# Optimization experiments

Hardware: AMD Instinct MI355X
Metric: run time of the kernel (lower is better)

The kernel has to match this reference:

```python
import jax, jax.numpy as jnp
import numpy as np

N = 8192          # total proposals
D_IN = 256 * 7 * 7  # 12544
HID = 1024
C = 3


def setup_inputs() -> dict:
    key = jax.random.key(0)
    ks = jax.random.split(key, 9)
    s_in = 1.0 / np.sqrt(D_IN)
    s_h = 1.0 / np.sqrt(HID)
    return {
        "feature_vectors": jax.random.normal(ks[0], (N, D_IN), dtype=jnp.float32),
        "W1": jax.random.uniform(ks[1], (D_IN, HID), jnp.float32, -s_in, s_in),
        "b1": jax.random.uniform(ks[2], (HID,), jnp.float32, -s_in, s_in),
        "W2": jax.random.uniform(ks[3], (HID, HID), jnp.float32, -s_h, s_h),
        "b2": jax.random.uniform(ks[4], (HID,), jnp.float32, -s_h, s_h),
        "Wc": jax.random.uniform(ks[5], (HID, C + 1), jnp.float32, -s_h, s_h),
        "bc": jax.random.uniform(ks[6], (C + 1,), jnp.float32, -s_h, s_h),
        "Wr": jax.random.uniform(ks[7], (HID, 4 * C), jnp.float32, -s_h, s_h),
        "br": jax.random.uniform(ks[8], (4 * C,), jnp.float32, -s_h, s_h),
    }


def reference(feature_vectors, W1, b1, W2, b2, Wc, bc, Wr, br):
    # intermediate: Linear -> Linear -> ReLU (note: no ReLU between the two Linears,
    # matching the original nn.Sequential ordering)
    h = feature_vectors @ W1 + b1          # [N, 1024]
    h = h @ W2 + b2                        # [N, 1024]
    h = jax.nn.relu(h)
    class_logits = jax.nn.softmax(h @ Wc + bc, axis=-1)  # [N, C+1]
    box_pred = h @ Wr + br                  # [N, 4C]
    return class_logits, box_pred
```

## Files before the change

kernel.cpp:

```cpp
#include <hip/hip_runtime.h>
#include <hip/hip_bf16.h>
#include <stdint.h>

using u16 = unsigned short;
using u32 = unsigned int;

typedef __attribute__((ext_vector_type(8))) short short8;
typedef __attribute__((ext_vector_type(4))) float floatx4;

__device__ __forceinline__ u16 f2bf(float f) {
  __hip_bfloat16 h = __float2bfloat16(f);
  return *reinterpret_cast<u16*>(&h);
}

__device__ __forceinline__ void gl_lds16(const void* g, void* l) {
  __builtin_amdgcn_global_load_lds((const __attribute__((address_space(1))) void*)g,
                                   (__attribute__((address_space(3))) void*)l, 16, 0, 0);
}

__global__ __launch_bounds__(256)
void transpose_to_bf16(const float* __restrict__ in, u16* __restrict__ out,
                       int R, int Cc) {
  __shared__ float tile[32][33];
  int c0 = blockIdx.x * 32;
  int r0 = blockIdx.y * 32;
  int tx = threadIdx.x;
  int ty = threadIdx.y;
#pragma unroll
  for (int i = 0; i < 32; i += 8)
    tile[ty + i][tx] = in[(size_t)(r0 + ty + i) * Cc + c0 + tx];
  __syncthreads();
#pragma unroll
  for (int i = 0; i < 32; i += 8)
    out[(size_t)(c0 + ty + i) * R + r0 + tx] = f2bf(tile[tx][ty + i]);
}

__global__ __launch_bounds__(256)
void cvt_bf16(const float4* __restrict__ in, uint2* __restrict__ out, int n4) {
  int i = blockIdx.x * 256 + threadIdx.x;
  if (i >= n4) return;
  float4 v = in[i];
  u32 lo = (u32)f2bf(v.x) | ((u32)f2bf(v.y) << 16);
  u32 hi = (u32)f2bf(v.z) | ((u32)f2bf(v.w) << 16);
  out[i] = make_uint2(lo, hi);
}

constexpr int BM = 128, BN = 128, BK = 32;

template <bool A_BF16, bool RELU>
__global__ __launch_bounds__(256, 3)
void gemm_bt(const void* __restrict__ Aip, const u16* __restrict__ BT,
             const float* __restrict__ bias, u16* __restrict__ C,
             int M, int N, int K) {
  __shared__ __align__(16) u16 As[BM * BK];
  __shared__ __align__(16) u16 Bs[BN * BK];
  const int tid  = threadIdx.x;
  const int lane = tid & 63;
  const int wave = tid >> 6;
  const int m0 = blockIdx.y * BM;
  const int n0 = blockIdx.x * BN;
  const int wm = (wave & 1) * 64;
  const int wn = (wave >> 1) * 64;
  const int row = lane & 15;
  const int kq  = lane >> 4;

  floatx4 acc[4][4] = {};

  int a_off[4], b_off[4];
#pragma unroll
  for (int t = 0; t < 4; ++t) {
    int mr = wm + t * 16 + row;
    a_off[t] = mr * BK + ((kq ^ ((mr >> 1) & 3)) * 8);
    int nr = wn + t * 16 + row;
    b_off[t] = nr * BK + ((kq ^ ((nr >> 1) & 3)) * 8);
  }

  const u16* bptr[2];
  int b_lds[2];
#pragma unroll
  for (int it = 0; it < 2; ++it) {
    int c = it * 256 + tid;
    int nrow = c >> 2;
    int kc = ((c & 3) ^ ((nrow >> 1) & 3)) * 8;
    bptr[it] = BT + (size_t)(n0 + nrow) * K + kc;
    b_lds[it] = (it * 256 + wave * 64) * 8;
  }

  const u16* aptrB[2];
  int a_ldsB[2];
  const float* aptrF[4];
  int a_stF[4];
  if constexpr (A_BF16) {
    const u16* A = (const u16*)Aip;
#pragma unroll
    for (int it = 0; it < 2; ++it) {
      int c = it * 256 + tid;
      int mrow = c >> 2;
      int kc = ((c & 3) ^ ((mrow >> 1) & 3)) * 8;
      aptrB[it] = A + (size_t)(m0 + mrow) * K + kc;
      a_ldsB[it] = (it * 256 + wave * 64) * 8;
    }
  } else {
    const float* A = (const float*)Aip;
#pragma unroll
    for (int it = 0; it < 4; ++it) {
      int idx = it * 256 + tid;
      int mrow = idx >> 3;
      int kc = (idx & 7) * 4;
      aptrF[it] = A + (size_t)(m0 + mrow) * K + kc;
      int chunk = kc >> 3, half = (kc >> 2) & 1;
      int sc = chunk ^ ((mrow >> 1) & 3);
      a_stF[it] = mrow * BK + sc * 8 + half * 4;
    }
  }

  for (int k0 = 0; k0 < K; k0 += BK) {
    __syncthreads();
    if constexpr (A_BF16) {
#pragma unroll
      for (int it = 0; it < 2; ++it)
        gl_lds16(aptrB[it] + k0, &As[a_ldsB[it]]);
    } else {
#pragma unroll
      for (int it = 0; it < 4; ++it) {
        float4 v = *(const float4*)(aptrF[it] + k0);
        u32 lo = (u32)f2bf(v.x) | ((u32)f2bf(v.y) << 16);
        u32 hi = (u32)f2bf(v.z) | ((u32)f2bf(v.w) << 16);
        *(uint2*)&As[a_stF[it]] = make_uint2(lo, hi);
      }
    }
#pragma unroll
    for (int it = 0; it < 2; ++it)
      gl_lds16(bptr[it] + k0, &Bs[b_lds[it]]);
    __syncthreads();

    short8 a[4], b[4];
#pragma unroll
    for (int t = 0; t < 4; ++t) {
      a[t] = *(const short8*)&As[a_off[t]];
      b[t] = *(const short8*)&Bs[b_off[t]];
    }
#pragma unroll
    for (int mt = 0; mt < 4; ++mt)
#pragma unroll
      for (int nt = 0; nt < 4; ++nt)
        acc[mt][nt] = __builtin_amdgcn_mfma_f32_16x16x32_bf16(
            a[mt], b[nt], acc[mt][nt], 0, 0, 0);
  }

  const int ccol = row;
  const int crow = kq * 4;
#pragma unroll
  for (int mt = 0; mt < 4; ++mt) {
#pragma unroll
    for (int nt = 0; nt < 4; ++nt) {
      int gm = m0 + wm + mt * 16 + crow;
      int gn = n0 + wn + nt * 16 + ccol;
      float bv = bias[gn];
#pragma unroll
      for (int r = 0; r < 4; ++r) {
        float v = acc[mt][nt][r] + bv;
        if (RELU) v = fmaxf(v, 0.f);
        C[(size_t)(gm + r) * N + gn] = f2bf(v);
      }
    }
  }
}

__device__ __forceinline__ float wave_sum(float v) {
#pragma unroll
  for (int m = 32; m >= 1; m >>= 1) v += __shfl_xor(v, m, 64);
  return v;
}

__global__ __launch_bounds__(64)
void head_kernel(const u16* __restrict__ H, const float* __restrict__ Wc,
                 const float* __restrict__ bc, const float* __restrict__ Wr,
                 const float* __restrict__ br, float* __restrict__ out) {
  const int rowi = blockIdx.x;
  const int lane = threadIdx.x;
  const u16* h = H + (size_t)rowi * 1024 + lane * 16;
  uint4 p0 = *(const uint4*)h;
  uint4 p1 = *(const uint4*)(h + 8);
  u32 w[8] = {p0.x, p0.y, p0.z, p0.w, p1.x, p1.y, p1.z, p1.w};
  float x[16];
#pragma unroll
  for (int i = 0; i < 8; ++i) {
    union { u32 u; float f; } lo, hi;
    lo.u = w[i] << 16;
    hi.u = w[i] & 0xffff0000u;
    x[2 * i] = lo.f;
    x[2 * i + 1] = hi.f;
  }
  float ac[4] = {};
  float ar[12] = {};
  const int kbase = lane * 16;
#pragma unroll
  for (int j = 0; j < 16; ++j) {
    float xv = x[j];
    const float* wc = Wc + (size_t)(kbase + j) * 4;
#pragma unroll
    for (int c = 0; c < 4; ++c) ac[c] = fmaf(xv, wc[c], ac[c]);
    const float* wr = Wr + (size_t)(kbase + j) * 12;
#pragma unroll
    for (int r = 0; r < 12; ++r) ar[r] = fmaf(xv, wr[r], ar[r]);
  }
#pragma unroll
  for (int c = 0; c < 4; ++c) ac[c] = wave_sum(ac[c]);
#pragma unroll
  for (int r = 0; r < 12; ++r) ar[r] = wave_sum(ar[r]);

  if (lane == 0) {
    float lg[4], mx = -1e30f;
#pragma unroll
    for (int c = 0; c < 4; ++c) { lg[c] = ac[c] + bc[c]; mx = fmaxf(mx, lg[c]); }
    float s = 0.f;
#pragma unroll
    for (int c = 0; c < 4; ++c) { lg[c] = __expf(lg[c] - mx); s += lg[c]; }
    float inv = 1.f / s;
#pragma unroll
    for (int c = 0; c < 4; ++c) out[(size_t)rowi * 4 + c] = lg[c] * inv;
    float* ob = out + 8192 * 4;
#pragma unroll
    for (int r = 0; r < 12; ++r) ob[(size_t)rowi * 12 + r] = ar[r] + br[r];
  }
}

extern "C" void kernel_launch(void* const* d_in, const int* in_sizes, int n_in,
                              void* d_out, int out_size, void* d_ws, size_t ws_size,
                              hipStream_t stream) {
  const float* X  = (const float*)d_in[0];
  const float* W1 = (const float*)d_in[1];
  const float* b1 = (const float*)d_in[2];
  const float* W2 = (const float*)d_in[3];
  const float* b2 = (const float*)d_in[4];
  const float* Wc = (const float*)d_in[5];
  const float* bc = (const float*)d_in[6];
  const float* Wr = (const float*)d_in[7];
  const float* br = (const float*)d_in[8];

  constexpr int NP = 8192, DIN = 12544, HID = 1024;
  char* ws = (char*)d_ws;
  u16* W1T = (u16*)ws;
  u16* W2T = (u16*)(ws + (size_t)HID * DIN * 2);
  u16* H1  = (u16*)((char*)W2T + (size_t)HID * HID * 2);
  u16* Hb  = H1 + (size_t)NP * HID;
  u16* Xb  = Hb + (size_t)NP * HID;
  size_t need_base = (size_t)HID * DIN * 2 + (size_t)HID * HID * 2 +
                     2 * (size_t)NP * HID * 2;
  bool use_xbf = ws_size >= need_base + (size_t)NP * DIN * 2;

  transpose_to_bf16<<<dim3(HID / 32, DIN / 32), dim3(32, 8), 0, stream>>>(W1, W1T, DIN, HID);
  transpose_to_bf16<<<dim3(HID / 32, HID / 32), dim3(32, 8), 0, stream>>>(W2, W2T, HID, HID);

  if (use_xbf) {
    int n4 = NP * DIN / 4;
    cvt_bf16<<<(n4 + 255) / 256, 256, 0, stream>>>((const float4*)X, (uint2*)Xb, n4);
    gemm_bt<true, false><<<dim3(HID / BN, NP / BM), 256, 0, stream>>>(
        Xb, W1T, b1, H1, NP, HID, DIN);
  } else {
    gemm_bt<false, false><<<dim3(HID / BN, NP / BM), 256, 0, stream>>>(
        X, W1T, b1, H1, NP, HID, DIN);
  }
  gemm_bt<true, true><<<dim3(HID / BN, NP / BM), 256, 0, stream>>>(
      H1, W2T, b2, Hb, NP, HID, HID);
  head_kernel<<<NP, 64, 0, stream>>>(Hb, Wc, bc, Wr, br, (float*)d_out);
}
```

Measured before the change: 1.015 ms.

## Shrink GEMM M-tile, add XCD-aware block swizzle, drop separate X conversion pass

The GEMM tile drops from 128x128 to 64x128 and occupancy is raised to 4 blocks per CU. A 1D grid with an XCD-aware mapping makes blocks on the same XCD share A rows and the full set of N columns, which should help L2 reuse. The standalone fp32-to-bf16 pass over X is removed, so the first GEMM always reads fp32 X and converts it in registers, avoiding a full extra read and write of the large activation. The head kernel now packs 4 rows per 256-thread block. The costs are lower arithmetic intensity per tile and twice as many W1 reads across M-tiles.

```diff
diff --git a/kernel.cpp b/kernel.cpp
--- a/kernel.cpp
+++ b/kernel.cpp
@@ -35,20 +35,10 @@
     out[(size_t)(c0 + ty + i) * R + r0 + tx] = f2bf(tile[tx][ty + i]);
 }
 
-__global__ __launch_bounds__(256)
-void cvt_bf16(const float4* __restrict__ in, uint2* __restrict__ out, int n4) {
-  int i = blockIdx.x * 256 + threadIdx.x;
-  if (i >= n4) return;
-  float4 v = in[i];
-  u32 lo = (u32)f2bf(v.x) | ((u32)f2bf(v.y) << 16);
-  u32 hi = (u32)f2bf(v.z) | ((u32)f2bf(v.w) << 16);
-  out[i] = make_uint2(lo, hi);
-}
-
-constexpr int BM = 128, BN = 128, BK = 32;
+constexpr int BM = 64, BN = 128, BK = 32;
 
 template <bool A_BF16, bool RELU>
-__global__ __launch_bounds__(256, 3)
+__global__ __launch_bounds__(256, 4)
 void gemm_bt(const void* __restrict__ Aip, const u16* __restrict__ BT,
              const float* __restrict__ bias, u16* __restrict__ C,
              int M, int N, int K) {
@@ -57,22 +47,32 @@
   const int tid  = threadIdx.x;
   const int lane = tid & 63;
   const int wave = tid >> 6;
-  const int m0 = blockIdx.y * BM;
-  const int n0 = blockIdx.x * BN;
-  const int wm = (wave & 1) * 64;
+
+  const int b   = blockIdx.x;
+  const int xcd = b & 7;
+  const int t   = b >> 3;
+  const int col = t & 7;
+  const int rh  = t >> 3;
+  const int m0  = (xcd + (rh << 3)) * BM;
+  const int n0  = col * BN;
+
+  const int wm = (wave & 1) * 32;
   const int wn = (wave >> 1) * 64;
   const int row = lane & 15;
   const int kq  = lane >> 4;
 
-  floatx4 acc[4][4] = {};
-
-  int a_off[4], b_off[4];
-#pragma unroll
-  for (int t = 0; t < 4; ++t) {
-    int mr = wm + t * 16 + row;
-    a_off[t] = mr * BK + ((kq ^ ((mr >> 1) & 3)) * 8);
-    int nr = wn + t * 16 + row;
-    b_off[t] = nr * BK + ((kq ^ ((nr >> 1) & 3)) * 8);
+  floatx4 acc[2][4] = {};
+
+  int a_off[2], b_off[4];
+#pragma unroll
+  for (int tt = 0; tt < 2; ++tt) {
+    int mr = wm + tt * 16 + row;
+    a_off[tt] = mr * BK + ((kq ^ ((mr >> 1) & 3)) * 8);
+  }
+#pragma unroll
+  for (int tt = 0; tt < 4; ++tt) {
+    int nr = wn + tt * 16 + row;
+    b_off[tt] = nr * BK + ((kq ^ ((nr >> 1) & 3)) * 8);
   }
 
   const u16* bptr[2];
@@ -86,24 +86,21 @@
     b_lds[it] = (it * 256 + wave * 64) * 8;
   }
 
-  const u16* aptrB[2];
-  int a_ldsB[2];
-  const float* aptrF[4];
-  int a_stF[4];
+  const u16* aptrB = nullptr;
+  int a_ldsB = 0;
+  const float* aptrF[2];
+  int a_stF[2];
   if constexpr (A_BF16) {
     const u16* A = (const u16*)Aip;
-#pragma unroll
-    for (int it = 0; it < 2; ++it) {
-      int c = it * 256 + tid;
-      int mrow = c >> 2;
-      int kc = ((c & 3) ^ ((mrow >> 1) & 3)) * 8;
-      aptrB[it] = A + (size_t)(m0 + mrow) * K + kc;
-      a_ldsB[it] = (it * 256 + wave * 64) * 8;
-    }
+    int c = tid;
+    int mrow = c >> 2;
+    int kc = ((c & 3) ^ ((mrow >> 1) & 3)) * 8;
+    aptrB = A + (size_t)(m0 + mrow) * K + kc;
+    a_ldsB = (wave * 64) * 8;
   } else {
     const float* A = (const float*)Aip;
 #pragma unroll
-    for (int it = 0; it < 4; ++it) {
+    for (int it = 0; it < 2; ++it) {
       int idx = it * 256 + tid;
       int mrow = idx >> 3;
       int kc = (idx & 7) * 4;
@@ -117,12 +114,10 @@
   for (int k0 = 0; k0 < K; k0 += BK) {
     __syncthreads();
     if constexpr (A_BF16) {
-#pragma unroll
-      for (int it = 0; it < 2; ++it)
-        gl_lds16(aptrB[it] + k0, &As[a_ldsB[it]]);
+      gl_lds16(aptrB + k0, &As[a_ldsB]);
     } else {
 #pragma unroll
-      for (int it = 0; it < 4; ++it) {
+      for (int it = 0; it < 2; ++it) {
         float4 v = *(const float4*)(aptrF[it] + k0);
         u32 lo = (u32)f2bf(v.x) | ((u32)f2bf(v.y) << 16);
         u32 hi = (u32)f2bf(v.z) | ((u32)f2bf(v.w) << 16);
@@ -134,24 +129,23 @@
       gl_lds16(bptr[it] + k0, &Bs[b_lds[it]]);
     __syncthreads();
 
-    short8 a[4], b[4];
-#pragma unroll
-    for (int t = 0; t < 4; ++t) {
-      a[t] = *(const short8*)&As[a_off[t]];
-      b[t] = *(const short8*)&Bs[b_off[t]];
-    }
-#pragma unroll
-    for (int mt = 0; mt < 4; ++mt)
+    short8 a[2], bb[4];
+#pragma unroll
+    for (int tt = 0; tt < 2; ++tt) a[tt] = *(const short8*)&As[a_off[tt]];
+#pragma unroll
+    for (int tt = 0; tt < 4; ++tt) bb[tt] = *(const short8*)&Bs[b_off[tt]];
+#pragma unroll
+    for (int mt = 0; mt < 2; ++mt)
 #pragma unroll
       for (int nt = 0; nt < 4; ++nt)
         acc[mt][nt] = __builtin_amdgcn_mfma_f32_16x16x32_bf16(
-            a[mt], b[nt], acc[mt][nt], 0, 0, 0);
+            a[mt], bb[nt], acc[mt][nt], 0, 0, 0);
   }
 
   const int ccol = row;
   const int crow = kq * 4;
 #pragma unroll
-  for (int mt = 0; mt < 4; ++mt) {
+  for (int mt = 0; mt < 2; ++mt) {
 #pragma unroll
     for (int nt = 0; nt < 4; ++nt) {
       int gm = m0 + wm + mt * 16 + crow;
@@ -173,12 +167,12 @@
   return v;
 }
 
-__global__ __launch_bounds__(64)
+__global__ __launch_bounds__(256)
 void head_kernel(const u16* __restrict__ H, const float* __restrict__ Wc,
                  const float* __restrict__ bc, const float* __restrict__ Wr,
                  const float* __restrict__ br, float* __restrict__ out) {
-  const int rowi = blockIdx.x;
-  const int lane = threadIdx.x;
+  const int rowi = blockIdx.x * 4 + (threadIdx.x >> 6);
+  const int lane = threadIdx.x & 63;
   const u16* h = H + (size_t)rowi * 1024 + lane * 16;
   uint4 p0 = *(const uint4*)h;
   uint4 p1 = *(const uint4*)(h + 8);
@@ -245,24 +239,13 @@
   u16* W2T = (u16*)(ws + (size_t)HID * DIN * 2);
   u16* H1  = (u16*)((char*)W2T + (size_t)HID * HID * 2);
   u16* Hb  = H1 + (size_t)NP * HID;
-  u16* Xb  = Hb + (size_t)NP * HID;
-  size_t need_base = (size_t)HID * DIN * 2 + (size_t)HID * HID * 2 +
-                     2 * (size_t)NP * HID * 2;
-  bool use_xbf = ws_size >= need_base + (size_t)NP * DIN * 2;
 
   transpose_to_bf16<<<dim3(HID / 32, DIN / 32), dim3(32, 8), 0, stream>>>(W1, W1T, DIN, HID);
   transpose_to_bf16<<<dim3(HID / 32, HID / 32), dim3(32, 8), 0, stream>>>(W2, W2T, HID, HID);
 
-  if (use_xbf) {
-    int n4 = NP * DIN / 4;
-    cvt_bf16<<<(n4 + 255) / 256, 256, 0, stream>>>((const float4*)X, (uint2*)Xb, n4);
-    gemm_bt<true, false><<<dim3(HID / BN, NP / BM), 256, 0, stream>>>(
-        Xb, W1T, b1, H1, NP, HID, DIN);
-  } else {
-    gemm_bt<false, false><<<dim3(HID / BN, NP / BM), 256, 0, stream>>>(
-        X, W1T, b1, H1, NP, HID, DIN);
-  }
-  gemm_bt<true, true><<<dim3(HID / BN, NP / BM), 256, 0, stream>>>(
+  gemm_bt<false, false><<<(NP / BM) * (HID / BN), 256, 0, stream>>>(
+      X, W1T, b1, H1, NP, HID, DIN);
+  gemm_bt<true, true><<<(NP / BM) * (HID / BN), 256, 0, stream>>>(
       H1, W2T, b2, Hb, NP, HID, HID);
-  head_kernel<<<NP, 64, 0, stream>>>(Hb, Wc, bc, Wr, br, (float*)d_out);
-}
+  head_kernel<<<NP / 4, 256, 0, stream>>>(Hb, Wc, bc, Wr, br, (float*)d_out);
+}
```

After: 1.058 ms. 1.04x slower.
